# Kernel optimization log

Hardware: AMD Instinct MI355X
Metric: run time of the kernel (lower is better)

## Reference

```python
import jax, jax.numpy as jnp
import numpy as np
import math

TAU = 0.07
KD_T = 3.0
MOM = 0.5
POS_K = 1
NEG_K = 8192


def _kldiv(y_s, y_t, T):
    # F.kl_div(log_softmax(y_s/T), softmax(y_t/T), 'batchmean') * T^2
    log_ps = jax.nn.log_softmax(y_s / T, axis=1)
    log_pt = jax.nn.log_softmax(y_t / T, axis=1)
    pt = jnp.exp(log_pt)
    return jnp.sum(pt * (log_pt - log_ps)) / y_s.shape[0] * (T * T)


def setup_inputs() -> dict:
    key = jax.random.key(0)
    ks = jax.random.split(key, 6)
    B, D, N = 128, 128, 100000
    stdv = 1.0 / math.sqrt(D / 3)
    emb0 = jax.random.normal(ks[0], (B, D), dtype=jnp.float32)
    emb0 = emb0 / jnp.linalg.norm(emb0, axis=1, keepdims=True)
    emb1 = jax.random.normal(ks[1], (B, D), dtype=jnp.float32)
    emb1 = emb1 / jnp.linalg.norm(emb1, axis=1, keepdims=True)
    mem0 = jax.random.uniform(ks[2], (N, D), minval=-stdv, maxval=stdv, dtype=jnp.float32)
    mem1 = jax.random.uniform(ks[3], (N, D), minval=-stdv, maxval=stdv, dtype=jnp.float32)
    pos_idx = jax.random.randint(ks[4], (B, POS_K + 1), 0, N)
    neg_idx = jax.random.randint(ks[5], (B, NEG_K), 0, N)
    return {"emb0": emb0, "emb1": emb1, "mem0": mem0, "mem1": mem1,
            "pos_idx": pos_idx, "neg_idx": neg_idx}


def _simi(mem, emb, idx):
    # gather [B,K,D] rows from memory bank (detached) and dot with emb [B,D]
    rep = jax.lax.stop_gradient(mem[idx])
    return jnp.einsum('bkd,bd->bk', rep, emb) / TAU


def reference(emb0, emb1, mem0, mem1, pos_idx, neg_idx):
    embs = [emb0, emb1]
    mems = [mem0, mem1]
    n_net = 2
    idx = jnp.concatenate([pos_idx, neg_idx], axis=1)  # [B, 1+pos_k+neg_k]

    # ---- inter (cross-network) logits + soft ICL loss ----
    inter_logits = []
    soft_icl = jnp.float32(0.0)
    for i in range(n_net):
        for j in range(i + 1, n_net):
            cij = _simi(mems[i], embs[j], idx)
            cji = _simi(mems[j], embs[i], idx)
            inter_logits += [cij, cji]
            soft_icl = soft_icl + _kldiv(cij, jax.lax.stop_gradient(cji), KD_T)
            soft_icl = soft_icl + _kldiv(cji, jax.lax.stop_gradient(cij), KD_T)

    npos = POS_K + 1
    icl = jnp.float32(0.0)
    for logit in inter_logits:
        lp = logit - jax.nn.logsumexp(logit, axis=1, keepdims=True)
        icl = icl + (-jnp.mean(jnp.sum(lp[:, :npos], axis=1) / npos))

    # ---- intra (within-network) logits ----
    idx2 = idx[:, 1:]  # drop the first positive
    intra_logits = [_simi(mems[i], embs[i], idx2) for i in range(n_net)]

    soft_vcl = jnp.float32(0.0)
    for i in range(n_net):
        for j in range(n_net):
            if i != j:
                soft_vcl = soft_vcl + _kldiv(intra_logits[i], jax.lax.stop_gradient(intra_logits[j]), KD_T)

    vcl = jnp.float32(0.0)
    for logit in intra_logits:
        lp = logit - jax.nn.logsumexp(logit, axis=1, keepdims=True)
        vcl = vcl + (-jnp.mean(jnp.sum(lp[:, :POS_K], axis=1) / POS_K))

    # ---- momentum update + L2 normalize + scatter back (no grad) ----
    p0 = pos_idx[:, 0]
    new_mems = []
    for i in range(n_net):
        pos = mems[i][p0]
        upd = MOM * pos + (1.0 - MOM) * embs[i]
        upd = upd / jnp.sqrt(jnp.sum(upd * upd, axis=1, keepdims=True))
        new_mems.append(jax.lax.stop_gradient(mems[i].at[p0].set(upd)))

    return (vcl, soft_vcl, icl, soft_icl, new_mems[0], new_mems[1])
```

## Files before the change

### kernel.cpp

```cpp
#include <hip/hip_runtime.h>
#include <math.h>

#define B 128
#define D 128
#define NMEM 100000
#define KTOT 8194
#define NEGK 8192
#define CHUNKS 16
#define CS 513

__global__ __launch_bounds__(256, 4) void gather_logits(
        const float* __restrict__ emb0, const float* __restrict__ emb1,
        const float* __restrict__ mem0, const float* __restrict__ mem1,
        const int* __restrict__ pos_idx, const int* __restrict__ neg_idx,
        float* __restrict__ partials) {
    const int c = blockIdx.x;
    const int b = blockIdx.y;
    const int tid = threadIdx.x;
    const int lane = tid & 63;
    const int w = tid >> 6;
    const int g = lane >> 3;
    const int l8 = lane & 7;
    const float INV_TAU = 1.0f / 0.07f;
    const float INV3 = 1.0f / 3.0f;

    float4 q0[4], q1[4];
    #pragma unroll
    for (int j = 0; j < 4; ++j) {
        q0[j] = *(const float4*)(emb0 + b * D + j * 32 + l8 * 4);
        q1[j] = *(const float4*)(emb1 + b * D + j * 32 + l8 * 4);
    }

    float s1ij = 0.f, s1ji = 0.f, s1i0 = 0.f, s1i1 = 0.f;
    float s3ij = 0.f, s3ji = 0.f, s3i0 = 0.f, s3i1 = 0.f;
    float wa = 0.f, wb = 0.f, wc = 0.f, wd = 0.f;

    __shared__ float red[4][12];
    __shared__ float sps[6];

    const int k0 = c * CS;
    const int kend = (k0 + CS < KTOT) ? k0 + CS : KTOT;
    const int kbase = k0 + w * 8 + g;
    const int posbase = b * 2;
    const int negbase = b * NEGK - 2;

    if (tid < 6) sps[tid] = 0.f;

    float4 A0[4], A1[4], B0[4], B1[4];

#define FETCH(IT, R0, R1) do {                                               \
    const int kf = kbase + (IT) * 32;                                        \
    const int kc = (kf < kend) ? kf : (kend - 1);                            \
    const int r = (kc < 2) ? pos_idx[posbase + kc] : neg_idx[negbase + kc];  \
    const float* p0 = mem0 + r * D + l8 * 4;                                 \
    const float* p1 = mem1 + r * D + l8 * 4;                                 \
    _Pragma("unroll")                                                        \
    for (int j = 0; j < 4; ++j) {                                            \
        R0[j] = *(const float4*)(p0 + j * 32);                               \
        R1[j] = *(const float4*)(p1 + j * 32);                               \
    }                                                                        \
} while (0)

#define COMPUTE(IT, R0, R1) do {                                             \
    const int kk = kbase + (IT) * 32;                                        \
    float pij = 0.f, pii = 0.f, pji = 0.f, pjj = 0.f;                        \
    _Pragma("unroll")                                                        \
    for (int j = 0; j < 4; ++j) {                                            \
        pij += R0[j].x * q1[j].x + R0[j].y * q1[j].y                         \
             + R0[j].z * q1[j].z + R0[j].w * q1[j].w;                        \
        pii += R0[j].x * q0[j].x + R0[j].y * q0[j].y                         \
             + R0[j].z * q0[j].z + R0[j].w * q0[j].w;                        \
        pji += R1[j].x * q0[j].x + R1[j].y * q0[j].y                         \
             + R1[j].z * q0[j].z + R1[j].w * q0[j].w;                        \
        pjj += R1[j].x * q1[j].x + R1[j].y * q1[j].y                         \
             + R1[j].z * q1[j].z + R1[j].w * q1[j].w;                        \
    }                                                                        \
    _Pragma("unroll")                                                        \
    for (int off = 1; off < 8; off <<= 1) {                                  \
        pij += __shfl_xor(pij, off, 64);                                     \
        pii += __shfl_xor(pii, off, 64);                                     \
        pji += __shfl_xor(pji, off, 64);                                     \
        pjj += __shfl_xor(pjj, off, 64);                                     \
    }                                                                        \
    const float mA = (kk < kend) ? 1.f : 0.f;                                \
    const float mI = (kk >= 1) ? mA : 0.f;                                   \
    const float cij = pij * INV_TAU, ci0 = pii * INV_TAU;                    \
    const float cji = pji * INV_TAU, ci1 = pjj * INV_TAU;                    \
    const float e3ij = __expf(cij * INV3), e3ji = __expf(cji * INV3);        \
    const float e3i0 = __expf(ci0 * INV3), e3i1 = __expf(ci1 * INV3);        \
    s1ij += mA * __expf(cij);                                                \
    s1ji += mA * __expf(cji);                                                \
    s3ij += mA * e3ij;                                                       \
    s3ji += mA * e3ji;                                                       \
    wa += mA * e3ji * (cji - cij);                                           \
    wb += mA * e3ij * (cij - cji);                                           \
    s1i0 += mI * __expf(ci0);                                                \
    s1i1 += mI * __expf(ci1);                                                \
    s3i0 += mI * e3i0;                                                       \
    s3i1 += mI * e3i1;                                                       \
    wc += mI * e3i1 * (ci1 - ci0);                                           \
    wd += mI * e3i0 * (ci0 - ci1);                                           \
    if (kk == 0 && l8 == 0) { sps[0] = cij; sps[2] = cji; }                  \
    if (kk == 1 && l8 == 0) { sps[1] = cij; sps[3] = cji;                    \
                              sps[4] = ci0; sps[5] = ci1; }                  \
} while (0)

    FETCH(0, A0, A1);
    for (int it = 0; it < 16; it += 2) {
        FETCH(it + 1, B0, B1);
        COMPUTE(it, A0, A1);
        FETCH(it + 2, A0, A1);
        COMPUTE(it + 1, B0, B1);
    }
    COMPUTE(16, A0, A1);

#undef FETCH
#undef COMPUTE

    float v[12] = {s1ij, s1ji, s1i0, s1i1, s3ij, s3ji, s3i0, s3i1, wa, wb, wc, wd};
    #pragma unroll
    for (int j = 0; j < 12; ++j) {
        v[j] += __shfl_xor(v[j], 8, 64);
        v[j] += __shfl_xor(v[j], 16, 64);
        v[j] += __shfl_xor(v[j], 32, 64);
    }
    if (lane == 0) {
        #pragma unroll
        for (int j = 0; j < 12; ++j) red[w][j] = v[j];
    }
    __syncthreads();
    float* outp = partials + (b * CHUNKS + c) * 20;
    if (tid < 12) outp[tid] = red[0][tid] + red[1][tid] + red[2][tid] + red[3][tid];
    else if (tid < 18) outp[tid] = sps[tid - 12];
}

__global__ void finalize(const float* __restrict__ partials, float* __restrict__ out) {
    const int b = threadIdx.x;
    float a[12];
    #pragma unroll
    for (int j = 0; j < 12; ++j) a[j] = 0.f;
    for (int c = 0; c < CHUNKS; ++c) {
        const float* p = partials + (b * CHUNKS + c) * 20;
        #pragma unroll
        for (int j = 0; j < 12; ++j) a[j] += p[j];
    }
    const float* e = partials + (b * CHUNKS) * 20 + 12;
    const float cij0 = e[0], cij1 = e[1], cji0 = e[2], cji1 = e[3], i01 = e[4], i11 = e[5];
    const float icl_b = -((cij0 + cij1) * 0.5f - __logf(a[0]))
                        - ((cji0 + cji1) * 0.5f - __logf(a[1]));
    const float vcl_b = -(i01 - __logf(a[2])) - (i11 - __logf(a[3]));
    const float sicl_b = 3.0f * (a[8] / a[5] + a[9] / a[4]);
    const float svcl_b = 3.0f * (a[10] / a[7] + a[11] / a[6]);
    __shared__ float r[4][128];
    r[0][b] = vcl_b; r[1][b] = svcl_b; r[2][b] = icl_b; r[3][b] = sicl_b;
    __syncthreads();
    for (int s = 64; s > 0; s >>= 1) {
        if (b < s) {
            r[0][b] += r[0][b + s]; r[1][b] += r[1][b + s];
            r[2][b] += r[2][b + s]; r[3][b] += r[3][b + s];
        }
        __syncthreads();
    }
    if (b == 0) {
        out[0] = r[0][0] * (1.0f / 128.f);
        out[1] = r[1][0] * (1.0f / 128.f);
        out[2] = r[2][0] * (1.0f / 128.f);
        out[3] = r[3][0] * (1.0f / 128.f);
    }
}

__global__ void copy_mems(const float4* __restrict__ m0, const float4* __restrict__ m1,
                          float4* __restrict__ o0, float4* __restrict__ o1) {
    const int n4 = NMEM * D / 4;
    for (int i = blockIdx.x * blockDim.x + threadIdx.x; i < n4; i += gridDim.x * blockDim.x) {
        o0[i] = m0[i];
        o1[i] = m1[i];
    }
}

__global__ void update_rows(const float* __restrict__ emb0, const float* __restrict__ emb1,
                            const float* __restrict__ mem0, const float* __restrict__ mem1,
                            const int* __restrict__ pos_idx,
                            float* __restrict__ o0, float* __restrict__ o1) {
    const int b = blockIdx.x;
    const int tid = threadIdx.x;
    const int lane = tid & 63;
    const int net = tid >> 6;
    const int p0 = pos_idx[b * 2];
    bool skip = false;
    for (int b2 = b + 1; b2 < B; ++b2)
        if (pos_idx[b2 * 2] == p0) skip = true;
    if (skip) return;
    const float* mem = net ? mem1 : mem0;
    const float* emb = net ? emb1 : emb0;
    float* o = net ? o1 : o0;
    const float2 mv = *(const float2*)(mem + p0 * D + 2 * lane);
    const float2 ev = *(const float2*)(emb + b * D + 2 * lane);
    const float ux = 0.5f * mv.x + 0.5f * ev.x;
    const float uy = 0.5f * mv.y + 0.5f * ev.y;
    float ss = ux * ux + uy * uy;
    #pragma unroll
    for (int off = 1; off < 64; off <<= 1) ss += __shfl_xor(ss, off, 64);
    const float inv = 1.0f / sqrtf(ss);
    float2 wv; wv.x = ux * inv; wv.y = uy * inv;
    *(float2*)(o + p0 * D + 2 * lane) = wv;
}

extern "C" void kernel_launch(void* const* d_in, const int* in_sizes, int n_in,
                              void* d_out, int out_size, void* d_ws, size_t ws_size,
                              hipStream_t stream) {
    const float* emb0 = (const float*)d_in[0];
    const float* emb1 = (const float*)d_in[1];
    const float* mem0 = (const float*)d_in[2];
    const float* mem1 = (const float*)d_in[3];
    const int* pos_idx = (const int*)d_in[4];
    const int* neg_idx = (const int*)d_in[5];
    float* out = (float*)d_out;
    float* partials = (float*)d_ws;

    float* out_m0 = out + 4;
    float* out_m1 = out + 4 + NMEM * D;

    gather_logits<<<dim3(CHUNKS, B), 256, 0, stream>>>(emb0, emb1, mem0, mem1,
                                                       pos_idx, neg_idx, partials);
    finalize<<<1, 128, 0, stream>>>(partials, out);
    copy_mems<<<4096, 256, 0, stream>>>((const float4*)mem0, (const float4*)mem1,
                                        (float4*)out_m0, (float4*)out_m1);
    update_rows<<<B, 128, 0, stream>>>(emb0, emb1, mem0, mem1, pos_idx, out_m0, out_m1);
}
```

Before: 339.6 us.

## Fuse memory-bank copy into gather kernel and merge finalize with row update

The full copy of both memory banks into the output is interleaved into the gather/logits kernel's fetch-compute loop as seven strided nontemporal float4 copy steps per thread. The finalize reduction and the momentum row update are merged into one kernel launch, with the last block doing the reduction. This removes two launches and overlaps the streaming copy with the latency-bound random gather, at the cost of more memory traffic competing inside the gather loop and extra register pressure.

```diff
diff --git a/kernel.cpp b/kernel.cpp
--- a/kernel.cpp
+++ b/kernel.cpp
@@ -8,12 +8,17 @@
 #define NEGK 8192
 #define CHUNKS 16
 #define CS 513
-
-__global__ __launch_bounds__(256, 4) void gather_logits(
+#define N4 (NMEM * D / 4)
+#define NTHREADS_TOTAL (CHUNKS * B * 256)
+
+typedef float nt4 __attribute__((ext_vector_type(4)));
+
+__global__ __launch_bounds__(256, 4) void gather_copy(
         const float* __restrict__ emb0, const float* __restrict__ emb1,
         const float* __restrict__ mem0, const float* __restrict__ mem1,
         const int* __restrict__ pos_idx, const int* __restrict__ neg_idx,
-        float* __restrict__ partials) {
+        float* __restrict__ partials,
+        float* __restrict__ out_m0, float* __restrict__ out_m1) {
     const int c = blockIdx.x;
     const int b = blockIdx.y;
     const int tid = threadIdx.x;
@@ -43,6 +48,12 @@
     const int kbase = k0 + w * 8 + g;
     const int posbase = b * 2;
     const int negbase = b * NEGK - 2;
+
+    const int cbase = (b * CHUNKS + c) * 256 + tid;
+    const nt4* cm0 = (const nt4*)mem0;
+    const nt4* cm1 = (const nt4*)mem1;
+    nt4* co0 = (nt4*)out_m0;
+    nt4* co1 = (nt4*)out_m1;
 
     if (tid < 6) sps[tid] = 0.f;
 
@@ -105,9 +116,21 @@
                               sps[4] = ci0; sps[5] = ci1; }                  \
 } while (0)
 
+#define COPYSTEP(S) do {                                                     \
+    const int ci = (S) * NTHREADS_TOTAL + cbase;                             \
+    if (ci < N4) {                                                           \
+        nt4 ca = __builtin_nontemporal_load(cm0 + ci);                       \
+        nt4 cb = __builtin_nontemporal_load(cm1 + ci);                       \
+        __builtin_nontemporal_store(ca, co0 + ci);                           \
+        __builtin_nontemporal_store(cb, co1 + ci);                           \
+    }                                                                        \
+} while (0)
+
     FETCH(0, A0, A1);
     for (int it = 0; it < 16; it += 2) {
         FETCH(it + 1, B0, B1);
+        const int s = it >> 1;
+        if (s < 7) COPYSTEP(s);
         COMPUTE(it, A0, A1);
         FETCH(it + 2, A0, A1);
         COMPUTE(it + 1, B0, B1);
@@ -116,6 +139,7 @@
 
 #undef FETCH
 #undef COMPUTE
+#undef COPYSTEP
 
     float v[12] = {s1ij, s1ji, s1i0, s1i1, s3ij, s3ji, s3i0, s3i1, wa, wb, wc, wd};
     #pragma unroll
@@ -134,7 +158,36 @@
     else if (tid < 18) outp[tid] = sps[tid - 12];
 }
 
-__global__ void finalize(const float* __restrict__ partials, float* __restrict__ out) {
+__global__ void final_update(const float* __restrict__ partials, float* __restrict__ out,
+                             const float* __restrict__ emb0, const float* __restrict__ emb1,
+                             const float* __restrict__ mem0, const float* __restrict__ mem1,
+                             const int* __restrict__ pos_idx,
+                             float* __restrict__ o0, float* __restrict__ o1) {
+    if (blockIdx.x < B) {
+        const int b = blockIdx.x;
+        const int tid = threadIdx.x;
+        const int lane = tid & 63;
+        const int net = tid >> 6;
+        const int p0 = pos_idx[b * 2];
+        bool skip = false;
+        for (int b2 = b + 1; b2 < B; ++b2)
+            if (pos_idx[b2 * 2] == p0) skip = true;
+        if (skip) return;
+        const float* mem = net ? mem1 : mem0;
+        const float* emb = net ? emb1 : emb0;
+        float* o = net ? o1 : o0;
+        const float2 mv = *(const float2*)(mem + p0 * D + 2 * lane);
+        const float2 ev = *(const float2*)(emb + b * D + 2 * lane);
+        const float ux = 0.5f * mv.x + 0.5f * ev.x;
+        const float uy = 0.5f * mv.y + 0.5f * ev.y;
+        float ss = ux * ux + uy * uy;
+        #pragma unroll
+        for (int off = 1; off < 64; off <<= 1) ss += __shfl_xor(ss, off, 64);
+        const float inv = 1.0f / sqrtf(ss);
+        float2 wv; wv.x = ux * inv; wv.y = uy * inv;
+        *(float2*)(o + p0 * D + 2 * lane) = wv;
+        return;
+    }
     const int b = threadIdx.x;
     float a[12];
     #pragma unroll
@@ -169,43 +222,6 @@
     }
 }
 
-__global__ void copy_mems(const float4* __restrict__ m0, const float4* __restrict__ m1,
-                          float4* __restrict__ o0, float4* __restrict__ o1) {
-    const int n4 = NMEM * D / 4;
-    for (int i = blockIdx.x * blockDim.x + threadIdx.x; i < n4; i += gridDim.x * blockDim.x) {
-        o0[i] = m0[i];
-        o1[i] = m1[i];
-    }
-}
-
-__global__ void update_rows(const float* __restrict__ emb0, const float* __restrict__ emb1,
-                            const float* __restrict__ mem0, const float* __restrict__ mem1,
-                            const int* __restrict__ pos_idx,
-                            float* __restrict__ o0, float* __restrict__ o1) {
-    const int b = blockIdx.x;
-    const int tid = threadIdx.x;
-    const int lane = tid & 63;
-    const int net = tid >> 6;
-    const int p0 = pos_idx[b * 2];
-    bool skip = false;
-    for (int b2 = b + 1; b2 < B; ++b2)
-        if (pos_idx[b2 * 2] == p0) skip = true;
-    if (skip) return;
-    const float* mem = net ? mem1 : mem0;
-    const float* emb = net ? emb1 : emb0;
-    float* o = net ? o1 : o0;
-    const float2 mv = *(const float2*)(mem + p0 * D + 2 * lane);
-    const float2 ev = *(const float2*)(emb + b * D + 2 * lane);
-    const float ux = 0.5f * mv.x + 0.5f * ev.x;
-    const float uy = 0.5f * mv.y + 0.5f * ev.y;
-    float ss = ux * ux + uy * uy;
-    #pragma unroll
-    for (int off = 1; off < 64; off <<= 1) ss += __shfl_xor(ss, off, 64);
-    const float inv = 1.0f / sqrtf(ss);
-    float2 wv; wv.x = ux * inv; wv.y = uy * inv;
-    *(float2*)(o + p0 * D + 2 * lane) = wv;
-}
-
 extern "C" void kernel_launch(void* const* d_in, const int* in_sizes, int n_in,
                               void* d_out, int out_size, void* d_ws, size_t ws_size,
                               hipStream_t stream) {
@@ -221,10 +237,9 @@
     float* out_m0 = out + 4;
     float* out_m1 = out + 4 + NMEM * D;
 
-    gather_logits<<<dim3(CHUNKS, B), 256, 0, stream>>>(emb0, emb1, mem0, mem1,
-                                                       pos_idx, neg_idx, partials);
-    finalize<<<1, 128, 0, stream>>>(partials, out);
-    copy_mems<<<4096, 256, 0, stream>>>((const float4*)mem0, (const float4*)mem1,
-                                        (float4*)out_m0, (float4*)out_m1);
-    update_rows<<<B, 128, 0, stream>>>(emb0, emb1, mem0, mem1, pos_idx, out_m0, out_m1);
+    gather_copy<<<dim3(CHUNKS, B), 256, 0, stream>>>(emb0, emb1, mem0, mem1,
+                                                     pos_idx, neg_idx, partials,
+                                                     out_m0, out_m1);
+    final_update<<<B + 1, 128, 0, stream>>>(partials, out, emb0, emb1,
+                                            mem0, mem1, pos_idx, out_m0, out_m1);
 }
```

Result: slower. 495.8 us (+46.0%).
